# Kernel tuning notes

Measured on AMD Instinct MI355X. Metric: run time of the kernel, lower is better.

Reference implementation:

```python
import jax, jax.numpy as jnp
import numpy as np

GRID = 32          # grid_size -> N = 1024 patches
NPT = 1            # num_prefix_tokens
SCALE = 8.0        # sqrt(dim_head=64)
EPS = 1e-5         # nn.LayerNorm default eps


def _ln(x, g, b):
    m = jnp.mean(x, axis=-1, keepdims=True)
    v = jnp.var(x, axis=-1, keepdims=True)
    return (x - m) / jnp.sqrt(v + EPS) * g + b


def setup_inputs() -> dict:
    key = jax.random.key(0)
    ks = jax.random.split(key, 12)
    B, T, D, Dh = 32, GRID * GRID + NPT, 768, 64
    s = 0.02
    return {
        "x": jax.random.normal(ks[0], (B, T, D), jnp.float32),
        "Wq": jax.random.normal(ks[1], (D, Dh), jnp.float32) * s,
        "Wk": jax.random.normal(ks[2], (D, Dh), jnp.float32) * s,
        "Wv": jax.random.normal(ks[3], (D, Dh), jnp.float32) * s,
        "gq": jnp.ones((Dh,), jnp.float32),
        "bq": jnp.zeros((Dh,), jnp.float32),
        "gk": jnp.ones((Dh,), jnp.float32),
        "bk": jnp.zeros((Dh,), jnp.float32),
        "Wsig": jax.random.normal(ks[4], (Dh, 2), jnp.float32) * s,
        "bsig": jnp.zeros((2,), jnp.float32),
        "Wa": jax.random.normal(ks[5], (Dh, 1), jnp.float32) * s,
        "ba": jnp.zeros((1,), jnp.float32),
    }


def reference(x, Wq, Wk, Wv, gq, bq, gk, bk, Wsig, bsig, Wa, ba):
    # x: [B, T, D] with T = GRID^2 + NPT
    q = _ln(x @ Wq, gq, bq)            # [B, T, Dh]
    k = _ln(x @ Wk, gk, bk)            # [B, T, Dh]
    v = x @ Wv                          # [B, T, Dh]

    q_patch = q[:, NPT:, :]             # [B, N, Dh]
    alpha = jax.nn.softplus(q_patch @ Wa + ba)[..., 0]   # [B, N]
    sig = jax.nn.sigmoid(q_patch @ Wsig + bsig)          # [B, N, 2]
    sx, sy = sig[..., 0], sig[..., 1]                     # [B, N] each

    # patch-grid relative displacements (vectorized replacement of the
    # O(N^2) python double loop)
    ii, jj = jnp.meshgrid(jnp.arange(GRID), jnp.arange(GRID), indexing="ij")
    coords = jnp.stack([ii.ravel(), jj.ravel()], axis=-1).astype(jnp.float32)  # [N,2]=(y,x)
    dy = coords[:, None, 0] - coords[None, :, 0]          # [N, N]
    dx = coords[:, None, 1] - coords[None, :, 1]          # [N, N]

    # Gaussian bias: G[b,p,q] = exp(-dx^2/(2 sx[b,p]^2) - dy^2/(2 sy[b,p]^2))
    G = jnp.exp(-(dx * dx) / (2.0 * sx[:, :, None] ** 2)
                - (dy * dy) / (2.0 * sy[:, :, None] ** 2))  # [B, N, N]
    S = alpha[:, :, None] * G                               # [B, N, N]

    sim = jnp.einsum("bqd,bkd->bqk", q, k)                  # [B, T, T]
    sim = sim.at[:, NPT:, NPT:].add(S)

    probs = jax.nn.softmax(sim / SCALE, axis=-1)
    return probs @ v                                         # [B, T, Dh]
```

## Files before the change

kernel.cpp:

```cpp
#include <hip/hip_runtime.h>
#include <hip/hip_bf16.h>
#include <math.h>

#define BDIM 32
#define TDIM 1025
#define DDIM 768
#define GRIDW 32
#define TPATCH 1024
#define SCALE 8.0f
#define EPSLN 1e-5f
#define NROW (BDIM * TDIM)
#define VTLD 1088
#define LDP  72
#define NTILES 17

typedef __attribute__((ext_vector_type(8))) short short8v;
typedef __attribute__((ext_vector_type(4))) float f32x4;

__device__ __forceinline__ unsigned short f2bf(float f) {
    unsigned int u = __float_as_uint(f);
    u += 0x7FFFu + ((u >> 16) & 1u);
    return (unsigned short)(u >> 16);
}

__device__ __forceinline__ short8v pack8(float4 a, float4 b) {
    union { short8v v; unsigned short s[8]; } u;
    u.s[0] = f2bf(a.x); u.s[1] = f2bf(a.y); u.s[2] = f2bf(a.z); u.s[3] = f2bf(a.w);
    u.s[4] = f2bf(b.x); u.s[5] = f2bf(b.y); u.s[6] = f2bf(b.z); u.s[7] = f2bf(b.w);
    return u.v;
}

template<int CTRL>
__device__ __forceinline__ float dpp_f(float x) {
    return __int_as_float(__builtin_amdgcn_update_dpp(
        __float_as_int(x), __float_as_int(x), CTRL, 0xF, 0xF, true));
}
__device__ __forceinline__ float red16_max(float x) {
    x = fmaxf(x, dpp_f<0xB1>(x));
    x = fmaxf(x, dpp_f<0x4E>(x));
    x = fmaxf(x, dpp_f<0x124>(x));
    x = fmaxf(x, dpp_f<0x128>(x));
    return x;
}
__device__ __forceinline__ float red16_sum(float x) {
    x += dpp_f<0xB1>(x);
    x += dpp_f<0x4E>(x);
    x += dpp_f<0x124>(x);
    x += dpp_f<0x128>(x);
    return x;
}

__global__ __launch_bounds__(256) void prep_w_kernel(
    const float* __restrict__ Wq, const float* __restrict__ Wk,
    const float* __restrict__ Wv, unsigned short* __restrict__ wT)
{
    const int c = blockIdx.x;
    const float* W = (c < 64) ? Wq : (c < 128) ? Wk : Wv;
    const int cc = c & 63;
    for (int k = threadIdx.x; k < DDIM; k += 256)
        wT[(size_t)c * DDIM + k] = f2bf(W[(size_t)k * 64 + cc]);
}

__global__ __launch_bounds__(256) void qkv_tile_kernel(
    const float* __restrict__ x, const unsigned short* __restrict__ wT,
    const float* __restrict__ gq, const float* __restrict__ bq,
    const float* __restrict__ gk, const float* __restrict__ bk,
    const float* __restrict__ Wsig, const float* __restrict__ bsig,
    const float* __restrict__ Wa, const float* __restrict__ ba,
    unsigned short* __restrict__ qb, unsigned short* __restrict__ kb,
    unsigned short* __restrict__ vb,
    float* __restrict__ a8, float* __restrict__ isx, float* __restrict__ isy)
{
    __shared__ unsigned short As[2][64][40];
    __shared__ unsigned short Bs[2][192][40];

    const int t  = threadIdx.x;
    const int wv = t >> 6;
    const int ln = t & 63;
    const int lq = ln >> 4;
    const int lr = ln & 15;
    const int tok0 = blockIdx.x * 64;

    const int arow = t >> 2;
    const int aseg = t & 3;
    const float* aptr = x + (size_t)min(tok0 + arow, NROW - 1) * DDIM + aseg * 8;
    const int brow = t >> 2;
    const int bseg = t & 3;

    f32x4 acc[12];
#pragma unroll
    for (int ni = 0; ni < 12; ++ni) acc[ni] = (f32x4){0.f, 0.f, 0.f, 0.f};

    float4 ra0, ra1;
    short8v rb0, rb1, rb2;

    ra0 = *(const float4*)(aptr + 0);
    ra1 = *(const float4*)(aptr + 4);
    rb0 = *(const short8v*)&wT[(size_t)(brow +   0) * DDIM + bseg * 8];
    rb1 = *(const short8v*)&wT[(size_t)(brow +  64) * DDIM + bseg * 8];
    rb2 = *(const short8v*)&wT[(size_t)(brow + 128) * DDIM + bseg * 8];

#pragma unroll
    for (int ks = 0; ks < 24; ++ks) {
        const int buf = ks & 1;
        *(short8v*)&As[buf][arow][aseg * 8]        = pack8(ra0, ra1);
        *(short8v*)&Bs[buf][brow +   0][bseg * 8]  = rb0;
        *(short8v*)&Bs[buf][brow +  64][bseg * 8]  = rb1;
        *(short8v*)&Bs[buf][brow + 128][bseg * 8]  = rb2;
        if (ks + 1 < 24) {
            const int k0 = (ks + 1) * 32;
            ra0 = *(const float4*)(aptr + k0 + 0);
            ra1 = *(const float4*)(aptr + k0 + 4);
            rb0 = *(const short8v*)&wT[(size_t)(brow +   0) * DDIM + k0 + bseg * 8];
            rb1 = *(const short8v*)&wT[(size_t)(brow +  64) * DDIM + k0 + bseg * 8];
            rb2 = *(const short8v*)&wT[(size_t)(brow + 128) * DDIM + k0 + bseg * 8];
        }
        __syncthreads();
        short8v af = *(const short8v*)&As[buf][wv * 16 + lr][lq * 8];
#pragma unroll
        for (int ni = 0; ni < 12; ++ni) {
            short8v bf = *(const short8v*)&Bs[buf][16 * ni + lr][lq * 8];
            acc[ni] = __builtin_amdgcn_mfma_f32_16x16x32_bf16(af, bf, acc[ni], 0, 0, 0);
        }
    }

    float gqv[4], bqv[4], gkv[4], bkv[4], wav[4], ws0[4], ws1[4];
#pragma unroll
    for (int ni = 0; ni < 4; ++ni) {
        int c = lr + 16 * ni;
        gqv[ni] = gq[c]; bqv[ni] = bq[c];
        gkv[ni] = gk[c]; bkv[ni] = bk[c];
        wav[ni] = Wa[c];
        ws0[ni] = Wsig[2 * c];
        ws1[ni] = Wsig[2 * c + 1];
    }
    const float ba0 = ba[0], bs0 = bsig[0], bs1 = bsig[1];

#pragma unroll
    for (int reg = 0; reg < 4; ++reg) {
        const int tokr = tok0 + wv * 16 + lq * 4 + reg;

        float s1 = 0.f, s2 = 0.f;
#pragma unroll
        for (int ni = 0; ni < 4; ++ni) {
            float v = acc[ni][reg];
            s1 += v; s2 += v * v;
        }
        s1 = red16_sum(s1);
        s2 = red16_sum(s2);
        float mean = s1 * (1.f / 64.f);
        float var  = s2 * (1.f / 64.f) - mean * mean;
        float rstd = rsqrtf(var + EPSLN);
        float qn[4];
#pragma unroll
        for (int ni = 0; ni < 4; ++ni)
            qn[ni] = (acc[ni][reg] - mean) * rstd * gqv[ni] + bqv[ni];

        s1 = 0.f; s2 = 0.f;
#pragma unroll
        for (int ni = 0; ni < 4; ++ni) {
            float v = acc[4 + ni][reg];
            s1 += v; s2 += v * v;
        }
        s1 = red16_sum(s1);
        s2 = red16_sum(s2);
        mean = s1 * (1.f / 64.f);
        var  = s2 * (1.f / 64.f) - mean * mean;
        rstd = rsqrtf(var + EPSLN);
        float kn[4];
#pragma unroll
        for (int ni = 0; ni < 4; ++ni)
            kn[ni] = (acc[4 + ni][reg] - mean) * rstd * gkv[ni] + bkv[ni];

        float da = 0.f, d0 = 0.f, d1 = 0.f;
#pragma unroll
        for (int ni = 0; ni < 4; ++ni) {
            da += qn[ni] * wav[ni];
            d0 += qn[ni] * ws0[ni];
            d1 += qn[ni] * ws1[ni];
        }
        da = red16_sum(da);
        d0 = red16_sum(d0);
        d1 = red16_sum(d1);

        if (tokr < NROW) {
            size_t base = (size_t)tokr * 64;
            int bidx = tokr / TDIM;
            int ti   = tokr - bidx * TDIM;
#pragma unroll
            for (int ni = 0; ni < 4; ++ni) {
                int c = lr + 16 * ni;
                qb[base + c] = f2bf(qn[ni]);
                kb[base + c] = f2bf(kn[ni]);
                vb[base + c] = f2bf(acc[8 + ni][reg]);
            }
            if (lr == 0 && ti >= 1) {
                int p = bidx * TPATCH + ti - 1;
                float av = da + ba0;
                float sp = (av > 20.f) ? av : log1pf(__expf(av));
                a8[p] = sp * (1.f / SCALE);
                float sx = 1.f / (1.f + __expf(-(d0 + bs0)));
                float sy = 1.f / (1.f + __expf(-(d1 + bs1)));
                isx[p] = 0.5f / (sx * sx);
                isy[p] = 0.5f / (sy * sy);
            }
        }
    }
}

__global__ __launch_bounds__(256) void vtrans_kernel(
    const unsigned short* __restrict__ vb, unsigned short* __restrict__ vT)
{
    __shared__ unsigned short tile[64][LDP];
    const int t  = threadIdx.x;
    const int bb = blockIdx.y;
    const int t0 = blockIdx.x * 64;

#pragma unroll
    for (int it = 0; it < 2; ++it) {
        int lin = t + it * 256;
        int tok = lin >> 3;
        int d0  = (lin & 7) * 8;
        short8v v8 = {0, 0, 0, 0, 0, 0, 0, 0};
        if (t0 + tok < TDIM)
            v8 = *(const short8v*)&vb[((size_t)bb * TDIM + t0 + tok) * 64 + d0];
        union { short8v v; unsigned short s[8]; } u; u.v = v8;
#pragma unroll
        for (int j = 0; j < 8; ++j) tile[d0 + j][tok] = u.s[j];
    }
    __syncthreads();

    const int dh = t >> 2;
    const int ch = t & 3;
    short8v o0 = *(const short8v*)&tile[dh][ch * 16];
    short8v o1 = *(const short8v*)&tile[dh][ch * 16 + 8];
    size_t dst = ((size_t)bb * 64 + dh) * VTLD + t0 + ch * 16;
    *(short8v*)&vT[dst]     = o0;
    *(short8v*)&vT[dst + 8] = o1;
}

__global__ __launch_bounds__(256) void attn_mfma_kernel(
    const unsigned short* __restrict__ qb, const unsigned short* __restrict__ kb,
    const unsigned short* __restrict__ vT,
    const float* __restrict__ a8, const float* __restrict__ isx,
    const float* __restrict__ isy, float* __restrict__ out)
{
    __shared__ unsigned short Ks[64][LDP];
    __shared__ unsigned short Vt[64][LDP];
    __shared__ unsigned short Pt[4][16][LDP];

    const int t  = threadIdx.x;
    const int wv = t >> 6;
    const int ln = t & 63;
    const int lq = ln >> 4;
    const int lr = ln & 15;
    const int bb = blockIdx.y;
    const int q0 = blockIdx.x * 64;

    const int qrow = min(q0 + wv * 16 + lr, TDIM - 1);
    const size_t qbase = ((size_t)bb * TDIM + qrow) * 64;
    const short8v aq0 = *(const short8v*)&qb[qbase + lq * 8];
    const short8v aq1 = *(const short8v*)&qb[qbase + 32 + lq * 8];

    float a8q[4], sxq[4], syq[4], qpy[4], qpx[4];
    bool  hasS[4];
#pragma unroll
    for (int reg = 0; reg < 4; ++reg) {
        int qg = q0 + wv * 16 + lq * 4 + reg;
        hasS[reg] = false;
        a8q[reg] = 0.f; sxq[reg] = 0.f; syq[reg] = 0.f; qpy[reg] = 0.f; qpx[reg] = 0.f;
        if (qg >= 1 && qg < TDIM) {
            int qp = qg - 1;
            hasS[reg] = true;
            a8q[reg] = a8 [bb * TPATCH + qp];
            sxq[reg] = isx[bb * TPATCH + qp];
            syq[reg] = isy[bb * TPATCH + qp];
            qpy[reg] = (float)(qp >> 5);
            qpx[reg] = (float)(qp & 31);
        }
    }

    float m[4]  = {-1e30f, -1e30f, -1e30f, -1e30f};
    float l[4]  = {0.f, 0.f, 0.f, 0.f};
    f32x4 oacc[4];
#pragma unroll
    for (int ni = 0; ni < 4; ++ni) oacc[ni] = (f32x4){0.f, 0.f, 0.f, 0.f};

    const int sk_row = t >> 3;
    const int sk_d0  = (t & 7) * 8;
    short8v rk[2], rv[2];
#pragma unroll
    for (int it = 0; it < 2; ++it) {
        int key = sk_row + 32 * it;
        rk[it] = (key < TDIM) ? *(const short8v*)&kb[((size_t)bb * TDIM + key) * 64 + sk_d0]
                              : (short8v){0,0,0,0,0,0,0,0};
        rv[it] = *(const short8v*)&vT[((size_t)bb * 64 + key) * VTLD + sk_d0];
    }

    for (int tile = 0; tile < NTILES; ++tile) {
        const int kt0 = tile * 64;
        __syncthreads();
#pragma unroll
        for (int it = 0; it < 2; ++it) {
            *(short8v*)&Ks[sk_row + 32 * it][sk_d0] = rk[it];
            *(short8v*)&Vt[sk_row + 32 * it][sk_d0] = rv[it];
        }
        if (tile + 1 < NTILES) {
            const int nk = kt0 + 64;
#pragma unroll
            for (int it = 0; it < 2; ++it) {
                int key = sk_row + 32 * it;
                int kg  = nk + key;
                rk[it] = (kg < TDIM) ? *(const short8v*)&kb[((size_t)bb * TDIM + kg) * 64 + sk_d0]
                                     : (short8v){0,0,0,0,0,0,0,0};
                rv[it] = *(const short8v*)&vT[((size_t)bb * 64 + key) * VTLD + nk + sk_d0];
            }
        }
        __syncthreads();

        f32x4 sac[4];
#pragma unroll
        for (int ni = 0; ni < 4; ++ni) sac[ni] = (f32x4){0.f, 0.f, 0.f, 0.f};
#pragma unroll
        for (int ni = 0; ni < 4; ++ni) {
            short8v b0 = *(const short8v*)&Ks[16 * ni + lr][lq * 8];
            short8v b1 = *(const short8v*)&Ks[16 * ni + lr][32 + lq * 8];
            sac[ni] = __builtin_amdgcn_mfma_f32_16x16x32_bf16(aq0, b0, sac[ni], 0, 0, 0);
            sac[ni] = __builtin_amdgcn_mfma_f32_16x16x32_bf16(aq1, b1, sac[ni], 0, 0, 0);
        }

#pragma unroll
        for (int ni = 0; ni < 4; ++ni) {
            int key = kt0 + 16 * ni + lr;
            int kp  = key - 1;
            float ky = (float)(kp >> 5);
            float kx = (float)(kp & 31);
            bool kvalid = (key >= 1) && (key < TDIM);
#pragma unroll
            for (int reg = 0; reg < 4; ++reg) {
                float z = sac[ni][reg] * (1.f / SCALE);
                if (kvalid && hasS[reg]) {
                    float dy = qpy[reg] - ky;
                    float dx = qpx[reg] - kx;
                    z += a8q[reg] * __expf(-(dx * dx * sxq[reg] + dy * dy * syq[reg]));
                }
                if (key >= TDIM) z = -1e30f;
                sac[ni][reg] = z;
            }
        }

        float scf[4];
#pragma unroll
        for (int reg = 0; reg < 4; ++reg) {
            float mx = fmaxf(fmaxf(sac[0][reg], sac[1][reg]),
                             fmaxf(sac[2][reg], sac[3][reg]));
            mx = red16_max(mx);
            float mn = fmaxf(m[reg], mx);
            scf[reg] = __expf(m[reg] - mn);
            m[reg] = mn;
            float ts = 0.f;
#pragma unroll
            for (int ni = 0; ni < 4; ++ni) {
                float pp = __expf(sac[ni][reg] - mn);
                sac[ni][reg] = pp;
                ts += pp;
            }
            ts = red16_sum(ts);
            l[reg] = l[reg] * scf[reg] + ts;
        }
#pragma unroll
        for (int ni = 0; ni < 4; ++ni)
#pragma unroll
            for (int reg = 0; reg < 4; ++reg)
                oacc[ni][reg] *= scf[reg];

#pragma unroll
        for (int ni = 0; ni < 4; ++ni)
#pragma unroll
            for (int reg = 0; reg < 4; ++reg)
                Pt[wv][lq * 4 + reg][16 * ni + lr] = f2bf(sac[ni][reg]);

#pragma unroll
        for (int ks = 0; ks < 2; ++ks) {
            short8v pa = *(const short8v*)&Pt[wv][lr][ks * 32 + lq * 8];
#pragma unroll
            for (int ni = 0; ni < 4; ++ni) {
                short8v bv = *(const short8v*)&Vt[16 * ni + lr][ks * 32 + lq * 8];
                oacc[ni] = __builtin_amdgcn_mfma_f32_16x16x32_bf16(pa, bv, oacc[ni], 0, 0, 0);
            }
        }
    }

#pragma unroll
    for (int reg = 0; reg < 4; ++reg) {
        int qg = q0 + wv * 16 + lq * 4 + reg;
        if (qg < TDIM) {
            float rl = 1.f / l[reg];
#pragma unroll
            for (int ni = 0; ni < 4; ++ni)
                out[((size_t)bb * TDIM + qg) * 64 + 16 * ni + lr] = oacc[ni][reg] * rl;
        }
    }
}

extern "C" void kernel_launch(void* const* d_in, const int* in_sizes, int n_in,
                              void* d_out, int out_size, void* d_ws, size_t ws_size,
                              hipStream_t stream)
{
    const float* x    = (const float*)d_in[0];
    const float* Wq   = (const float*)d_in[1];
    const float* Wk   = (const float*)d_in[2];
    const float* Wv   = (const float*)d_in[3];
    const float* gq   = (const float*)d_in[4];
    const float* bq   = (const float*)d_in[5];
    const float* gk   = (const float*)d_in[6];
    const float* bk   = (const float*)d_in[7];
    const float* Wsig = (const float*)d_in[8];
    const float* bsig = (const float*)d_in[9];
    const float* Wa   = (const float*)d_in[10];
    const float* ba   = (const float*)d_in[11];
    float* out = (float*)d_out;

    char* w = (char*)d_ws;
    const size_t NQ = (size_t)NROW * 64;
    unsigned short* qb = (unsigned short*)w;   w += NQ * 2;
    unsigned short* kb = (unsigned short*)w;   w += NQ * 2;
    unsigned short* vb = (unsigned short*)w;   w += NQ * 2;
    unsigned short* vT = (unsigned short*)w;   w += (size_t)BDIM * 64 * VTLD * 2;
    float* a8  = (float*)w;                    w += (size_t)BDIM * TPATCH * 4;
    float* isx = (float*)w;                    w += (size_t)BDIM * TPATCH * 4;
    float* isy = (float*)w;                    w += (size_t)BDIM * TPATCH * 4;
    unsigned short* wT = (unsigned short*)w;   w += (size_t)192 * DDIM * 2;

    hipLaunchKernelGGL(prep_w_kernel, dim3(192), dim3(256), 0, stream,
                       Wq, Wk, Wv, wT);

    const int nblk1 = (NROW + 63) / 64;
    hipLaunchKernelGGL(qkv_tile_kernel, dim3(nblk1), dim3(256), 0, stream,
                       x, wT, gq, bq, gk, bk, Wsig, bsig, Wa, ba,
                       qb, kb, vb, a8, isx, isy);

    hipLaunchKernelGGL(vtrans_kernel, dim3(17, BDIM), dim3(256), 0, stream,
                       vb, vT);

    hipLaunchKernelGGL(attn_mfma_kernel, dim3(17, BDIM), dim3(256), 0, stream,
                       qb, kb, vT, a8, isx, isy, out);
}
```

Measured before the change: 98.93 us.

## Double-buffer LDS tiles in QKV and attention kernels with one barrier per step

The QKV projection kernel now uses a K-step of 64 instead of 32, with wider LDS tiles and a double-buffered load/compute/store schedule. That halves the iteration count and leaves one barrier per step. The attention kernel likewise double-buffers its K and V tiles in LDS, storing the next tile after compute so only one __syncthreads is needed per tile instead of two. This aims to cut barrier stalls and overlap global loads with MFMA work, at the cost of more LDS and more registers, which may reduce occupancy.

```diff
diff --git a/kernel.cpp b/kernel.cpp
--- a/kernel.cpp
+++ b/kernel.cpp
@@ -71,8 +71,8 @@
     unsigned short* __restrict__ vb,
     float* __restrict__ a8, float* __restrict__ isx, float* __restrict__ isy)
 {
-    __shared__ unsigned short As[2][64][40];
-    __shared__ unsigned short Bs[2][192][40];
+    __shared__ unsigned short As[2][64][LDP];
+    __shared__ unsigned short Bs[2][192][LDP];
 
     const int t  = threadIdx.x;
     const int wv = t >> 6;
@@ -81,48 +81,71 @@
     const int lr = ln & 15;
     const int tok0 = blockIdx.x * 64;
 
-    const int arow = t >> 2;
-    const int aseg = t & 3;
-    const float* aptr = x + (size_t)min(tok0 + arow, NROW - 1) * DDIM + aseg * 8;
-    const int brow = t >> 2;
-    const int bseg = t & 3;
+    const float* la_ptr[2];
+    const unsigned short* lb_ptr[6];
+#pragma unroll
+    for (int j = 0; j < 2; ++j) {
+        int lin = t + 256 * j;
+        la_ptr[j] = x + (size_t)min(tok0 + (lin >> 3), NROW - 1) * DDIM + (lin & 7) * 8;
+    }
+#pragma unroll
+    for (int j = 0; j < 6; ++j) {
+        int lin = t + 256 * j;
+        lb_ptr[j] = wT + (size_t)(lin >> 3) * DDIM + (lin & 7) * 8;
+    }
+
+    float4  raf[2][2];
+    short8v rbv[6];
+
+#define QLOAD(K0)                                                              \
+    do {                                                                       \
+        _Pragma("unroll") for (int j = 0; j < 2; ++j) {                        \
+            raf[j][0] = *(const float4*)(la_ptr[j] + (K0));                    \
+            raf[j][1] = *(const float4*)(la_ptr[j] + (K0) + 4);                \
+        }                                                                      \
+        _Pragma("unroll") for (int j = 0; j < 6; ++j)                          \
+            rbv[j] = *(const short8v*)(lb_ptr[j] + (K0));                      \
+    } while (0)
+
+#define QSTORE(BUF)                                                            \
+    do {                                                                       \
+        _Pragma("unroll") for (int j = 0; j < 2; ++j) {                        \
+            int lin = t + 256 * j;                                             \
+            *(short8v*)&As[BUF][lin >> 3][(lin & 7) * 8] =                     \
+                pack8(raf[j][0], raf[j][1]);                                   \
+        }                                                                      \
+        _Pragma("unroll") for (int j = 0; j < 6; ++j) {                        \
+            int lin = t + 256 * j;                                             \
+            *(short8v*)&Bs[BUF][lin >> 3][(lin & 7) * 8] = rbv[j];             \
+        }                                                                      \
+    } while (0)
 
     f32x4 acc[12];
 #pragma unroll
     for (int ni = 0; ni < 12; ++ni) acc[ni] = (f32x4){0.f, 0.f, 0.f, 0.f};
 
-    float4 ra0, ra1;
-    short8v rb0, rb1, rb2;
-
-    ra0 = *(const float4*)(aptr + 0);
-    ra1 = *(const float4*)(aptr + 4);
-    rb0 = *(const short8v*)&wT[(size_t)(brow +   0) * DDIM + bseg * 8];
-    rb1 = *(const short8v*)&wT[(size_t)(brow +  64) * DDIM + bseg * 8];
-    rb2 = *(const short8v*)&wT[(size_t)(brow + 128) * DDIM + bseg * 8];
-
-#pragma unroll
-    for (int ks = 0; ks < 24; ++ks) {
+    QLOAD(0);
+    QSTORE(0);
+    __syncthreads();
+
+#pragma unroll
+    for (int ks = 0; ks < 12; ++ks) {
         const int buf = ks & 1;
-        *(short8v*)&As[buf][arow][aseg * 8]        = pack8(ra0, ra1);
-        *(short8v*)&Bs[buf][brow +   0][bseg * 8]  = rb0;
-        *(short8v*)&Bs[buf][brow +  64][bseg * 8]  = rb1;
-        *(short8v*)&Bs[buf][brow + 128][bseg * 8]  = rb2;
-        if (ks + 1 < 24) {
-            const int k0 = (ks + 1) * 32;
-            ra0 = *(const float4*)(aptr + k0 + 0);
-            ra1 = *(const float4*)(aptr + k0 + 4);
-            rb0 = *(const short8v*)&wT[(size_t)(brow +   0) * DDIM + k0 + bseg * 8];
-            rb1 = *(const short8v*)&wT[(size_t)(brow +  64) * DDIM + k0 + bseg * 8];
-            rb2 = *(const short8v*)&wT[(size_t)(brow + 128) * DDIM + k0 + bseg * 8];
-        }
+        if (ks + 1 < 12) QLOAD((ks + 1) * 64);
+        short8v af0 = *(const short8v*)&As[buf][wv * 16 + lr][lq * 8];
+        short8v af1 = *(const short8v*)&As[buf][wv * 16 + lr][32 + lq * 8];
+#pragma unroll
+        for (int ni = 0; ni < 12; ++ni) {
+            short8v bf0 = *(const short8v*)&Bs[buf][16 * ni + lr][lq * 8];
+            acc[ni] = __builtin_amdgcn_mfma_f32_16x16x32_bf16(af0, bf0, acc[ni], 0, 0, 0);
+            short8v bf1 = *(const short8v*)&Bs[buf][16 * ni + lr][32 + lq * 8];
+            acc[ni] = __builtin_amdgcn_mfma_f32_16x16x32_bf16(af1, bf1, acc[ni], 0, 0, 0);
+        }
+        if (ks + 1 < 12) QSTORE(buf ^ 1);
         __syncthreads();
-        short8v af = *(const short8v*)&As[buf][wv * 16 + lr][lq * 8];
-#pragma unroll
-        for (int ni = 0; ni < 12; ++ni) {
-            short8v bf = *(const short8v*)&Bs[buf][16 * ni + lr][lq * 8];
-            acc[ni] = __builtin_amdgcn_mfma_f32_16x16x32_bf16(af, bf, acc[ni], 0, 0, 0);
-        }
-    }
+    }
+#undef QLOAD
+#undef QSTORE
 
     float gqv[4], bqv[4], gkv[4], bkv[4], wav[4], ws0[4], ws1[4];
 #pragma unroll
@@ -245,8 +268,8 @@
     const float* __restrict__ a8, const float* __restrict__ isx,
     const float* __restrict__ isy, float* __restrict__ out)
 {
-    __shared__ unsigned short Ks[64][LDP];
-    __shared__ unsigned short Vt[64][LDP];
+    __shared__ unsigned short Ks[2][64][LDP];
+    __shared__ unsigned short Vt[2][64][LDP];
     __shared__ unsigned short Pt[4][16][LDP];
 
     const int t  = threadIdx.x;
@@ -289,42 +312,44 @@
     const int sk_row = t >> 3;
     const int sk_d0  = (t & 7) * 8;
     short8v rk[2], rv[2];
-#pragma unroll
-    for (int it = 0; it < 2; ++it) {
-        int key = sk_row + 32 * it;
-        rk[it] = (key < TDIM) ? *(const short8v*)&kb[((size_t)bb * TDIM + key) * 64 + sk_d0]
-                              : (short8v){0,0,0,0,0,0,0,0};
-        rv[it] = *(const short8v*)&vT[((size_t)bb * 64 + key) * VTLD + sk_d0];
-    }
+
+#define ALOAD(KT0)                                                             \
+    do {                                                                       \
+        _Pragma("unroll") for (int it = 0; it < 2; ++it) {                     \
+            int key = sk_row + 32 * it;                                        \
+            int kg  = (KT0) + key;                                             \
+            rk[it] = (kg < TDIM)                                               \
+                ? *(const short8v*)&kb[((size_t)bb * TDIM + kg) * 64 + sk_d0]  \
+                : (short8v){0, 0, 0, 0, 0, 0, 0, 0};                           \
+            rv[it] = *(const short8v*)&vT[((size_t)bb * 64 + key) * VTLD +     \
+                                          (KT0) + sk_d0];                      \
+        }                                                                      \
+    } while (0)
+
+#define ASTORE(BUF)                                                            \
+    do {                                                                       \
+        _Pragma("unroll") for (int it = 0; it < 2; ++it) {                     \
+            *(short8v*)&Ks[BUF][sk_row + 32 * it][sk_d0] = rk[it];             \
+            *(short8v*)&Vt[BUF][sk_row + 32 * it][sk_d0] = rv[it];             \
+        }                                                                      \
+    } while (0)
+
+    ALOAD(0);
+    ASTORE(0);
+    __syncthreads();
 
     for (int tile = 0; tile < NTILES; ++tile) {
         const int kt0 = tile * 64;
-        __syncthreads();
-#pragma unroll
-        for (int it = 0; it < 2; ++it) {
-            *(short8v*)&Ks[sk_row + 32 * it][sk_d0] = rk[it];
-            *(short8v*)&Vt[sk_row + 32 * it][sk_d0] = rv[it];
-        }
-        if (tile + 1 < NTILES) {
-            const int nk = kt0 + 64;
-#pragma unroll
-            for (int it = 0; it < 2; ++it) {
-                int key = sk_row + 32 * it;
-                int kg  = nk + key;
-                rk[it] = (kg < TDIM) ? *(const short8v*)&kb[((size_t)bb * TDIM + kg) * 64 + sk_d0]
-                                     : (short8v){0,0,0,0,0,0,0,0};
-                rv[it] = *(const short8v*)&vT[((size_t)bb * 64 + key) * VTLD + nk + sk_d0];
-            }
-        }
-        __syncthreads();
+        const int buf = tile & 1;
+        if (tile + 1 < NTILES) ALOAD(kt0 + 64);
 
         f32x4 sac[4];
 #pragma unroll
         for (int ni = 0; ni < 4; ++ni) sac[ni] = (f32x4){0.f, 0.f, 0.f, 0.f};
 #pragma unroll
         for (int ni = 0; ni < 4; ++ni) {
-            short8v b0 = *(const short8v*)&Ks[16 * ni + lr][lq * 8];
-            short8v b1 = *(const short8v*)&Ks[16 * ni + lr][32 + lq * 8];
+            short8v b0 = *(const short8v*)&Ks[buf][16 * ni + lr][lq * 8];
+            short8v b1 = *(const short8v*)&Ks[buf][16 * ni + lr][32 + lq * 8];
             sac[ni] = __builtin_amdgcn_mfma_f32_16x16x32_bf16(aq0, b0, sac[ni], 0, 0, 0);
             sac[ni] = __builtin_amdgcn_mfma_f32_16x16x32_bf16(aq1, b1, sac[ni], 0, 0, 0);
         }
@@ -385,11 +410,16 @@
             short8v pa = *(const short8v*)&Pt[wv][lr][ks * 32 + lq * 8];
 #pragma unroll
             for (int ni = 0; ni < 4; ++ni) {
-                short8v bv = *(const short8v*)&Vt[16 * ni + lr][ks * 32 + lq * 8];
+                short8v bv = *(const short8v*)&Vt[buf][16 * ni + lr][ks * 32 + lq * 8];
                 oacc[ni] = __builtin_amdgcn_mfma_f32_16x16x32_bf16(pa, bv, oacc[ni], 0, 0, 0);
             }
         }
-    }
+
+        if (tile + 1 < NTILES) ASTORE(buf ^ 1);
+        __syncthreads();
+    }
+#undef ALOAD
+#undef ASTORE
 
 #pragma unroll
     for (int reg = 0; reg < 4; ++reg) {
```

New measurement: 108.5 us. 1.1x slower.

## Double-buffer K/V shared tiles in attention with a single barrier per tile

Applied to the files above, without the earlier changes.

The attention kernel now keeps two LDS buffers for K and V. It writes the next tile into the alternate buffer after computing on the current one, so the per-tile pair of __syncthreads drops to one custom barrier that waits on lgkmcnt. In the QKV kernel, the DPP-based 16-lane reductions are replaced by __shfl_xor loops, and a padding constant is added for the existing LDS arrays. The double buffer doubles K/V LDS use, which may lower occupancy. The shuffle reductions may cost more instructions than the DPP versions they replace.

```diff
diff --git a/kernel.cpp b/kernel.cpp
--- a/kernel.cpp
+++ b/kernel.cpp
@@ -12,6 +12,7 @@
 #define NROW (BDIM * TDIM)
 #define VTLD 1088
 #define LDP  72
+#define LDQ  40
 #define NTILES 17
 
 typedef __attribute__((ext_vector_type(8))) short short8v;
@@ -28,6 +29,12 @@
     u.s[0] = f2bf(a.x); u.s[1] = f2bf(a.y); u.s[2] = f2bf(a.z); u.s[3] = f2bf(a.w);
     u.s[4] = f2bf(b.x); u.s[5] = f2bf(b.y); u.s[6] = f2bf(b.z); u.s[7] = f2bf(b.w);
     return u.v;
+}
+
+__device__ __forceinline__ void wg_barrier() {
+    asm volatile("s_waitcnt lgkmcnt(0)" ::: "memory");
+    __builtin_amdgcn_s_barrier();
+    __builtin_amdgcn_sched_barrier(0);
 }
 
 template<int CTRL>
@@ -71,8 +78,8 @@
     unsigned short* __restrict__ vb,
     float* __restrict__ a8, float* __restrict__ isx, float* __restrict__ isy)
 {
-    __shared__ unsigned short As[2][64][40];
-    __shared__ unsigned short Bs[2][192][40];
+    __shared__ unsigned short As[2][64][LDQ];
+    __shared__ unsigned short Bs[2][192][LDQ];
 
     const int t  = threadIdx.x;
     const int wv = t >> 6;
@@ -146,8 +153,11 @@
             float v = acc[ni][reg];
             s1 += v; s2 += v * v;
         }
-        s1 = red16_sum(s1);
-        s2 = red16_sum(s2);
+#pragma unroll
+        for (int off = 1; off < 16; off <<= 1) {
+            s1 += __shfl_xor(s1, off);
+            s2 += __shfl_xor(s2, off);
+        }
         float mean = s1 * (1.f / 64.f);
         float var  = s2 * (1.f / 64.f) - mean * mean;
         float rstd = rsqrtf(var + EPSLN);
@@ -162,8 +172,11 @@
             float v = acc[4 + ni][reg];
             s1 += v; s2 += v * v;
         }
-        s1 = red16_sum(s1);
-        s2 = red16_sum(s2);
+#pragma unroll
+        for (int off = 1; off < 16; off <<= 1) {
+            s1 += __shfl_xor(s1, off);
+            s2 += __shfl_xor(s2, off);
+        }
         mean = s1 * (1.f / 64.f);
         var  = s2 * (1.f / 64.f) - mean * mean;
         rstd = rsqrtf(var + EPSLN);
@@ -179,9 +192,12 @@
             d0 += qn[ni] * ws0[ni];
             d1 += qn[ni] * ws1[ni];
         }
-        da = red16_sum(da);
-        d0 = red16_sum(d0);
-        d1 = red16_sum(d1);
+#pragma unroll
+        for (int off = 1; off < 16; off <<= 1) {
+            da += __shfl_xor(da, off);
+            d0 += __shfl_xor(d0, off);
+            d1 += __shfl_xor(d1, off);
+        }
 
         if (tokr < NROW) {
             size_t base = (size_t)tokr * 64;
@@ -245,8 +261,8 @@
     const float* __restrict__ a8, const float* __restrict__ isx,
     const float* __restrict__ isy, float* __restrict__ out)
 {
-    __shared__ unsigned short Ks[64][LDP];
-    __shared__ unsigned short Vt[64][LDP];
+    __shared__ unsigned short Ks[2][64][LDP];
+    __shared__ unsigned short Vt[2][64][LDP];
     __shared__ unsigned short Pt[4][16][LDP];
 
     const int t  = threadIdx.x;
@@ -289,42 +305,44 @@
     const int sk_row = t >> 3;
     const int sk_d0  = (t & 7) * 8;
     short8v rk[2], rv[2];
-#pragma unroll
-    for (int it = 0; it < 2; ++it) {
-        int key = sk_row + 32 * it;
-        rk[it] = (key < TDIM) ? *(const short8v*)&kb[((size_t)bb * TDIM + key) * 64 + sk_d0]
-                              : (short8v){0,0,0,0,0,0,0,0};
-        rv[it] = *(const short8v*)&vT[((size_t)bb * 64 + key) * VTLD + sk_d0];
-    }
+
+#define ALOAD(KT0)                                                             \
+    do {                                                                       \
+        _Pragma("unroll") for (int it = 0; it < 2; ++it) {                     \
+            int key = sk_row + 32 * it;                                        \
+            int kg  = (KT0) + key;                                             \
+            rk[it] = (kg < TDIM)                                               \
+                ? *(const short8v*)&kb[((size_t)bb * TDIM + kg) * 64 + sk_d0]  \
+                : (short8v){0, 0, 0, 0, 0, 0, 0, 0};                           \
+            rv[it] = *(const short8v*)&vT[((size_t)bb * 64 + key) * VTLD +     \
+                                          (KT0) + sk_d0];                      \
+        }                                                                      \
+    } while (0)
+
+#define ASTORE(BUF)                                                            \
+    do {                                                                       \
+        _Pragma("unroll") for (int it = 0; it < 2; ++it) {                     \
+            *(short8v*)&Ks[BUF][sk_row + 32 * it][sk_d0] = rk[it];             \
+            *(short8v*)&Vt[BUF][sk_row + 32 * it][sk_d0] = rv[it];             \
+        }                                                                      \
+    } while (0)
+
+    ALOAD(0);
+    ASTORE(0);
+    wg_barrier();
 
     for (int tile = 0; tile < NTILES; ++tile) {
         const int kt0 = tile * 64;
-        __syncthreads();
-#pragma unroll
-        for (int it = 0; it < 2; ++it) {
-            *(short8v*)&Ks[sk_row + 32 * it][sk_d0] = rk[it];
-            *(short8v*)&Vt[sk_row + 32 * it][sk_d0] = rv[it];
-        }
-        if (tile + 1 < NTILES) {
-            const int nk = kt0 + 64;
-#pragma unroll
-            for (int it = 0; it < 2; ++it) {
-                int key = sk_row + 32 * it;
-                int kg  = nk + key;
-                rk[it] = (kg < TDIM) ? *(const short8v*)&kb[((size_t)bb * TDIM + kg) * 64 + sk_d0]
-                                     : (short8v){0,0,0,0,0,0,0,0};
-                rv[it] = *(const short8v*)&vT[((size_t)bb * 64 + key) * VTLD + nk + sk_d0];
-            }
-        }
-        __syncthreads();
+        const int buf = tile & 1;
+        if (tile + 1 < NTILES) ALOAD(kt0 + 64);
 
         f32x4 sac[4];
 #pragma unroll
         for (int ni = 0; ni < 4; ++ni) sac[ni] = (f32x4){0.f, 0.f, 0.f, 0.f};
 #pragma unroll
         for (int ni = 0; ni < 4; ++ni) {
-            short8v b0 = *(const short8v*)&Ks[16 * ni + lr][lq * 8];
-            short8v b1 = *(const short8v*)&Ks[16 * ni + lr][32 + lq * 8];
+            short8v b0 = *(const short8v*)&Ks[buf][16 * ni + lr][lq * 8];
+            short8v b1 = *(const short8v*)&Ks[buf][16 * ni + lr][32 + lq * 8];
             sac[ni] = __builtin_amdgcn_mfma_f32_16x16x32_bf16(aq0, b0, sac[ni], 0, 0, 0);
             sac[ni] = __builtin_amdgcn_mfma_f32_16x16x32_bf16(aq1, b1, sac[ni], 0, 0, 0);
         }
@@ -385,11 +403,16 @@
             short8v pa = *(const short8v*)&Pt[wv][lr][ks * 32 + lq * 8];
 #pragma unroll
             for (int ni = 0; ni < 4; ++ni) {
-                short8v bv = *(const short8v*)&Vt[16 * ni + lr][ks * 32 + lq * 8];
+                short8v bv = *(const short8v*)&Vt[buf][16 * ni + lr][ks * 32 + lq * 8];
                 oacc[ni] = __builtin_amdgcn_mfma_f32_16x16x32_bf16(pa, bv, oacc[ni], 0, 0, 0);
             }
         }
-    }
+
+        if (tile + 1 < NTILES) ASTORE(buf ^ 1);
+        wg_barrier();
+    }
+#undef ALOAD
+#undef ASTORE
 
 #pragma unroll
     for (int reg = 0; reg < 4; ++reg) {
```

After: 95.28 us. -3.7%, faster.
